# Optimization experiments

Measured on AMD Instinct MI355X. Metric: run time of the kernel, lower is better.

## Reference

```python
import math
import jax, jax.numpy as jnp
import numpy as np

B, L, E, H = 16, 4096, 512, 8
D = E // H
CORR_FACTOR = 2.0


def setup_inputs() -> dict:
    key = jax.random.key(0)
    ks = jax.random.split(key, 11)
    std = 1.0 / math.sqrt(E)
    mk = lambda k: (jax.random.normal(k, (E, E), jnp.float32) * std)
    return {
        "queries": jax.random.normal(ks[0], (B, L, E), jnp.float32),
        "keys": jax.random.normal(ks[1], (B, L, E), jnp.float32),
        "values": jax.random.normal(ks[2], (B, L, E), jnp.float32),
        "Wq": mk(ks[3]), "bq": jax.random.normal(ks[4], (E,), jnp.float32) * std,
        "Wk": mk(ks[5]), "bk": jax.random.normal(ks[6], (E,), jnp.float32) * std,
        "Wv": mk(ks[7]), "bv": jax.random.normal(ks[8], (E,), jnp.float32) * std,
        "Wo": mk(ks[9]), "bo": jax.random.normal(ks[10], (E,), jnp.float32) * std,
    }


def reference(queries, keys, values, Wq, bq, Wk, bk, Wv, bv, Wo, bo):
    # Projections (torch nn.Linear: x @ W.T + b), then split heads and move
    # to (B, H, D, L) layout used by the FFT / aggregation stages.
    def proj(x, W, b):
        y = x @ W.T + b                      # (B, L, E)
        return y.reshape(B, L, H, D).transpose(0, 2, 3, 1)  # (B, H, D, L)

    Q = proj(queries, Wq, bq)
    K = proj(keys, Wk, bk)
    V = proj(values, Wv, bv)

    # --- auto-correlation via Wiener-Khinchin (O(L log L)) ---
    qf = jnp.fft.rfft(Q, axis=-1)
    kf = jnp.fft.rfft(K, axis=-1)
    corr = jnp.fft.irfft(qf * jnp.conj(kf), n=L, axis=-1)  # (B, H, D, L)

    k_top = int(CORR_FACTOR * math.log(L))   # = 16
    corr_mean = jnp.mean(corr, axis=(1, 2))  # (B, L)
    top_vals, top_delays = jax.lax.top_k(corr_mean, k_top)  # (B, k)
    probs = jax.nn.softmax(top_vals, axis=-1)               # (B, k)

    pos = jnp.arange(L)
    agg = jnp.zeros_like(V)
    for i in range(k_top):  # small fixed loop over top-k delays
        idx = (pos[None, :] + top_delays[:, i:i + 1]) % L   # (B, L); == tiled gather
        v_del = jnp.take_along_axis(V, idx[:, None, None, :], axis=-1)
        agg = agg + probs[:, i, None, None, None] * v_del

    ctx = agg.transpose(0, 3, 1, 2).reshape(B, L, E)  # combine heads
    return ctx @ Wo.T + bo
```

## Files before the change

kernel.cpp:

```cpp
#include <hip/hip_runtime.h>
#include <hip/hip_bf16.h>
#include <math.h>


#define B_ 16
#define L_ 4096
#define E_ 512
#define NCAND 18
#define KTOP 16

typedef __attribute__((ext_vector_type(8))) short bf16x8;
typedef __attribute__((ext_vector_type(4))) float f32x4;

__device__ __forceinline__ float2 cmul(float2 a, float2 b) {
  return make_float2(a.x*b.x - a.y*b.y, a.x*b.y + a.y*b.x);
}
__device__ __forceinline__ float2 cadd(float2 a, float2 b){return make_float2(a.x+b.x, a.y+b.y);}
__device__ __forceinline__ float2 csub(float2 a, float2 b){return make_float2(a.x-b.x, a.y-b.y);}
__device__ __forceinline__ float2 cnegi(float2 a){return make_float2(a.y, -a.x);}
__device__ __forceinline__ unsigned short bf16_rne(float x) {
  unsigned int u = __float_as_uint(x);
  unsigned int r = u + 0x7FFFu + ((u >> 16) & 1u);
  return (unsigned short)(r >> 16);
}
__device__ __forceinline__ float bf16_f(unsigned short h) {
  return __uint_as_float(((unsigned int)h) << 16);
}

__device__ __forceinline__ void dft4(float2 a, float2 b, float2 c, float2 d,
                                     float2& X0, float2& X1, float2& X2, float2& X3) {
  float2 t0 = cadd(a,c), t1 = csub(a,c), t2 = cadd(b,d), t3 = csub(b,d);
  X0 = cadd(t0, t2); X2 = csub(t0, t2);
  float2 it3 = cnegi(t3);
  X1 = cadd(t1, it3);
  X3 = csub(t1, it3);
}

__device__ __forceinline__ void dft16(float2* v) {
  float2 B[4][4];
#pragma unroll
  for (int p = 0; p < 4; ++p)
    dft4(v[p], v[p+4], v[p+8], v[p+12], B[p][0], B[p][1], B[p][2], B[p][3]);
  const float C1 = 0.92387953251128674f, S1 = 0.38268343236508978f;
  const float C2 = 0.70710678118654752f;
  B[1][1] = cmul(B[1][1], make_float2( C1, -S1));
  B[1][2] = cmul(B[1][2], make_float2( C2, -C2));
  B[1][3] = cmul(B[1][3], make_float2( S1, -C1));
  B[2][1] = cmul(B[2][1], make_float2( C2, -C2));
  B[2][2] = cnegi(B[2][2]);
  B[2][3] = cmul(B[2][3], make_float2(-C2, -C2));
  B[3][1] = cmul(B[3][1], make_float2( S1, -C1));
  B[3][2] = cmul(B[3][2], make_float2(-C2, -C2));
  B[3][3] = cmul(B[3][3], make_float2(-C1,  S1));
#pragma unroll
  for (int r = 0; r < 4; ++r)
    dft4(B[0][r], B[1][r], B[2][r], B[3][r], v[r], v[r+4], v[r+8], v[r+12]);
}

__device__ __forceinline__ void fft4096_stages(float2* buf, int tid,
                                               const float2* __restrict__ tw) {
  float2 z[16];
#pragma unroll
  for (int q = 0; q < 16; ++q) z[q] = buf[tid + 256*q];
  __syncthreads();
  dft16(z);
  {
    const int p = tid, pa = tid & 15;
    buf[p*16 + (0 ^ pa)] = z[0];
#pragma unroll
    for (int r = 1; r < 16; ++r)
      buf[p*16 + (r ^ pa)] = cmul(z[r], tw[p*r]);
  }
  __syncthreads();
  {
    const int a = tid >> 4, r = tid & 15;
    float2 v[16];
#pragma unroll
    for (int bb = 0; bb < 16; ++bb) v[bb] = buf[(a + 16*bb)*16 + (r ^ a)];
    __syncthreads();
    dft16(v);
    buf[a*256 + 0*16 + r] = v[0];
#pragma unroll
    for (int c = 1; c < 16; ++c)
      buf[a*256 + c*16 + r] = cmul(v[c], tw[16*a*c]);
  }
  __syncthreads();
  {
    float2 y[16];
#pragma unroll
    for (int a = 0; a < 16; ++a) y[a] = buf[256*a + tid];
    __syncthreads();
    dft16(y);
#pragma unroll
    for (int d = 0; d < 16; ++d) buf[tid + 256*d] = y[d];
  }
  __syncthreads();
}

template<bool SPLIT>
__global__ __launch_bounds__(256) void conv_tile(
    const float* __restrict__ Xsrc,
    unsigned short* __restrict__ Thi, unsigned short* __restrict__ Tlo)
{
  const int bx = blockIdx.x;
  const int t  = blockIdx.y;
  const int tid = threadIdx.x;
  const int r = tid >> 1;
  const int h = tid & 1;
  const float* src = Xsrc + ((size_t)(bx*128 + r))*512 + t*32 + h*16;
  float xa[16];
#pragma unroll
  for (int q = 0; q < 4; ++q) {
    float4 v = *reinterpret_cast<const float4*>(src + 4*q);
    xa[4*q+0]=v.x; xa[4*q+1]=v.y; xa[4*q+2]=v.z; xa[4*q+3]=v.w;
  }
  size_t base = ((size_t)(bx*16 + t))*4096;
#pragma unroll
  for (int c = 0; c < 2; ++c) {
    int lk = h*2 + c;
    bf16x8 vh, vl;
#pragma unroll
    for (int e = 0; e < 8; ++e) {
      unsigned short hh = bf16_rne(xa[c*8+e]);
      vh[e] = (short)hh;
      if (SPLIT) vl[e] = (short)bf16_rne(xa[c*8+e] - bf16_f(hh));
    }
    *reinterpret_cast<bf16x8*>(Thi + base + ((size_t)lk*128 + r)*8) = vh;
    if (SPLIT)
      *reinterpret_cast<bf16x8*>(Tlo + base + ((size_t)lk*128 + r)*8) = vl;
  }
}

__global__ __launch_bounds__(256, 4) void gemm_qk(
    const float* __restrict__ Xq, const float* __restrict__ Xk,
    const unsigned short* __restrict__ Wqhi, const unsigned short* __restrict__ Wqlo,
    const unsigned short* __restrict__ Wkhi, const unsigned short* __restrict__ Wklo,
    const float* __restrict__ bq, const float* __restrict__ bk,
    float* __restrict__ Yq, float* __restrict__ Yk)
{
  __shared__ unsigned short Xh[2][2048], Xl[2][2048];
  const int sel = blockIdx.z;
  const float* X = sel ? Xk : Xq;
  const unsigned short* Whi = sel ? Wkhi : Wqhi;
  const unsigned short* Wlo = sel ? Wklo : Wqlo;
  const float* bias = sel ? bk : bq;
  float* Y = sel ? Yk : Yq;

  const int tid  = threadIdx.x;
  const int ny   = blockIdx.x;
  const int lt   = blockIdx.y;
  const int wave = tid >> 6;
  const int lane = tid & 63;
  const int lr   = lane & 15;
  const int lk   = lane >> 4;
  const int n0   = ny*256 + wave*64;
  const int cr   = tid >> 2;
  const int ch   = tid & 3;
  const int t0   = ((lt << 1) | ny) & 15;

  f32x4 acc[4][4];
#pragma unroll
  for (int i = 0; i < 4; ++i)
#pragma unroll
    for (int j = 0; j < 4; ++j) acc[i][j] = (f32x4){0.f,0.f,0.f,0.f};

  const float* Xb = X + ((size_t)(lt*64 + cr))*512 + ch*8;

  for (int it = 0; it < 16; ++it) {
    const int t = (t0 + it) & 15;
    const int p = it & 1;
    {
      float4 v0 = *reinterpret_cast<const float4*>(Xb + t*32);
      float4 v1 = *reinterpret_cast<const float4*>(Xb + t*32 + 4);
      float xa[8] = {v0.x,v0.y,v0.z,v0.w,v1.x,v1.y,v1.z,v1.w};
      bf16x8 vh, vl;
#pragma unroll
      for (int e = 0; e < 8; ++e) {
        unsigned short hh = bf16_rne(xa[e]);
        vh[e] = (short)hh;
        vl[e] = (short)bf16_rne(xa[e] - bf16_f(hh));
      }
      int u = (ch*64 + cr) ^ (ch*2);
      *reinterpret_cast<bf16x8*>(&Xh[p][u*8]) = vh;
      *reinterpret_cast<bf16x8*>(&Xl[p][u*8]) = vl;
    }
    bf16x8 ah[4], al[4];
#pragma unroll
    for (int i = 0; i < 4; ++i) {
      int n = n0 + i*16 + lr;
      size_t o = ((size_t)((n>>7)*16 + t))*4096 + ((size_t)lk*128 + (n&127))*8;
      ah[i] = *reinterpret_cast<const bf16x8*>(Whi + o);
      al[i] = *reinterpret_cast<const bf16x8*>(Wlo + o);
    }
    __syncthreads();

    __builtin_amdgcn_s_setprio(1);
#pragma unroll
    for (int j = 0; j < 4; ++j) {
      int u = (lk*64 + (j*16 + lr)) ^ (lk*2);
      bf16x8 bh = *reinterpret_cast<const bf16x8*>(&Xh[p][u*8]);
      bf16x8 bl = *reinterpret_cast<const bf16x8*>(&Xl[p][u*8]);
#pragma unroll
      for (int i = 0; i < 4; ++i) {
        acc[i][j] = __builtin_amdgcn_mfma_f32_16x16x32_bf16(ah[i], bh, acc[i][j], 0, 0, 0);
        acc[i][j] = __builtin_amdgcn_mfma_f32_16x16x32_bf16(ah[i], bl, acc[i][j], 0, 0, 0);
        acc[i][j] = __builtin_amdgcn_mfma_f32_16x16x32_bf16(al[i], bh, acc[i][j], 0, 0, 0);
      }
    }
    __builtin_amdgcn_s_setprio(0);
  }

  const int bb = lt >> 6;
  const int lbase = (lt & 63)*64;
#pragma unroll
  for (int i = 0; i < 4; ++i) {
    int n = n0 + i*16 + lk*4;
#pragma unroll
    for (int j = 0; j < 4; ++j) {
      int l = lbase + j*16 + lr;
#pragma unroll
      for (int r = 0; r < 4; ++r) {
        Y[((size_t)(bb*512 + n + r))*4096 + l] = acc[i][j][r] + bias[n + r];
      }
    }
  }
}

__global__ __launch_bounds__(512) void gemm_ov(
    const float* __restrict__ V, const unsigned short* __restrict__ Wct,
    const float* __restrict__ bias, unsigned short* __restrict__ Y16)
{
  __shared__ unsigned short Vs[2][256*8];
  const int tid  = threadIdx.x;
  const int bx   = blockIdx.x;
  const int wave = tid >> 6;
  const int lane = tid & 63;
  const int lr   = lane & 15;
  const int lk   = lane >> 4;
  const int n0   = wave*64;
  const int cr   = tid >> 3;
  const int ch   = tid & 7;
  const int clk  = ch >> 1;
  const int chh  = ch & 1;
  const int coff = (((clk*64 + cr) ^ clk)*8 + chh*4);
  const int t0   = bx & 15;

  f32x4 acc[4][4];
#pragma unroll
  for (int i = 0; i < 4; ++i)
#pragma unroll
    for (int j = 0; j < 4; ++j) acc[i][j] = (f32x4){0.f,0.f,0.f,0.f};

  const float* Vb = V + (size_t)bx*64*512 + (size_t)cr*512 + ch*4;
  float4 xv = *reinterpret_cast<const float4*>(Vb + t0*32);

  for (int it = 0; it < 16; ++it) {
    const int t = (t0 + it) & 15;
    const int p = it & 1;
    uint2 hi2 = make_uint2(
        (unsigned)bf16_rne(xv.x) | ((unsigned)bf16_rne(xv.y) << 16),
        (unsigned)bf16_rne(xv.z) | ((unsigned)bf16_rne(xv.w) << 16));
    *reinterpret_cast<uint2*>(&Vs[p][coff]) = hi2;
    float4 xnext;
    if (it < 15) {
      int tn = (t0 + it + 1) & 15;
      xnext = *reinterpret_cast<const float4*>(Vb + tn*32);
    }
    __syncthreads();

    bf16x8 av[4];
#pragma unroll
    for (int i = 0; i < 4; ++i) {
      int u = ((lk*64 + i*16 + lr) ^ lk)*8;
      av[i] = *reinterpret_cast<const bf16x8*>(&Vs[p][u]);
    }
#pragma unroll
    for (int j = 0; j < 4; ++j) {
      int n = n0 + j*16 + lr;
      size_t o = ((size_t)((n>>7)*16 + t))*4096 + ((size_t)lk*128 + (n&127))*8;
      bf16x8 bw = *reinterpret_cast<const bf16x8*>(Wct + o);
#pragma unroll
      for (int i = 0; i < 4; ++i)
        acc[i][j] = __builtin_amdgcn_mfma_f32_16x16x32_bf16(av[i], bw, acc[i][j], 0, 0, 0);
    }
    if (it < 15) xv = xnext;
  }

#pragma unroll
  for (int i = 0; i < 4; ++i) {
#pragma unroll
    for (int j = 0; j < 4; ++j) {
      int n = n0 + j*16 + lr;
      float bs = bias[n];
#pragma unroll
      for (int r = 0; r < 4; ++r) {
        int m = bx*64 + i*16 + lk*4 + r;
        Y16[(size_t)m*512 + n] = bf16_rne(acc[i][j][r] + bs);
      }
    }
  }
}

__global__ __launch_bounds__(256) void combine_kernel(
    const float* __restrict__ Wo, const float* __restrict__ Wv,
    const float* __restrict__ bv, const float* __restrict__ bo,
    float* __restrict__ Wc, float* __restrict__ bc)
{
  int n = blockIdx.x;
  int tid = threadIdx.x;
  float a0 = 0.f, a1 = 0.f;
  for (int j = 0; j < 512; ++j) {
    float wo = Wo[(size_t)n*512 + j];
    a0 += wo * Wv[(size_t)j*512 + tid];
    a1 += wo * Wv[(size_t)j*512 + tid + 256];
  }
  Wc[(size_t)n*512 + tid]       = a0;
  Wc[(size_t)n*512 + tid + 256] = a1;

  float p = 0.f;
  for (int j = tid; j < 512; j += 256) p += Wo[(size_t)n*512 + j] * bv[j];
  __shared__ float red[256];
  red[tid] = p; __syncthreads();
  for (int off = 128; off > 0; off >>= 1) {
    if (tid < off) red[tid] += red[tid + off];
    __syncthreads();
  }
  if (tid == 0) bc[n] = red[0] + bo[n];
}

__global__ void init_tw_kernel(float2* __restrict__ tw) {
  int k = blockIdx.x * 256 + threadIdx.x;
  if (k < 4096) {
    double ang = -2.0 * M_PI * (double)k / 4096.0;
    tw[k] = make_float2((float)cos(ang), (float)sin(ang));
  }
}

template<int CHB>
__global__ __launch_bounds__(256) void fft_corr_kernel(
    const float* __restrict__ Qt, const float* __restrict__ Kt,
    const float2* __restrict__ tw, float2* __restrict__ Spart)
{
  __shared__ float2 buf[4096];
  const int NG = 512 / CHB;
  const int b = blockIdx.x / NG;
  const int g = blockIdx.x % NG;
  const int tid = threadIdx.x;

  float2 acc[16];
#pragma unroll
  for (int m = 0; m < 16; ++m) acc[m] = make_float2(0.f, 0.f);

  float4 qv[4], kv[4];
  {
    const float* Qr = Qt + ((size_t)b*512 + g*CHB) * 4096;
    const float* Kr = Kt + ((size_t)b*512 + g*CHB) * 4096;
#pragma unroll
    for (int j = 0; j < 4; ++j) {
      qv[j] = *reinterpret_cast<const float4*>(Qr + 4*(tid + 256*j));
      kv[j] = *reinterpret_cast<const float4*>(Kr + 4*(tid + 256*j));
    }
  }

  for (int cc = 0; cc < CHB; ++cc) {
#pragma unroll
    for (int j = 0; j < 4; ++j) {
      int l0 = 4*(tid + 256*j);
      buf[l0+0] = make_float2(qv[j].x, kv[j].x);
      buf[l0+1] = make_float2(qv[j].y, kv[j].y);
      buf[l0+2] = make_float2(qv[j].z, kv[j].z);
      buf[l0+3] = make_float2(qv[j].w, kv[j].w);
    }
    __syncthreads();
    if (cc + 1 < CHB) {
      const float* Qr = Qt + ((size_t)b*512 + g*CHB + cc + 1) * 4096;
      const float* Kr = Kt + ((size_t)b*512 + g*CHB + cc + 1) * 4096;
#pragma unroll
      for (int j = 0; j < 4; ++j) {
        qv[j] = *reinterpret_cast<const float4*>(Qr + 4*(tid + 256*j));
        kv[j] = *reinterpret_cast<const float4*>(Kr + 4*(tid + 256*j));
      }
    }

    fft4096_stages(buf, tid, tw);

#pragma unroll
    for (int m = 0; m < 16; ++m) {
      int f = tid + 256*m;
      float2 zf = buf[f];
      float2 zm = buf[(4096 - f) & 4095];
      float2 qf = make_float2(0.5f*(zf.x + zm.x), 0.5f*(zf.y - zm.y));
      float2 df = make_float2(0.5f*(zf.x - zm.x), 0.5f*(zf.y + zm.y));
      float2 kf = make_float2(df.y, -df.x);
      acc[m].x += qf.x*kf.x + qf.y*kf.y;
      acc[m].y += qf.y*kf.x - qf.x*kf.y;
    }
    __syncthreads();
  }
  float2* Sp = Spart + ((size_t)(b*NG + g)) * 4096;
#pragma unroll
  for (int m = 0; m < 16; ++m) Sp[tid + 256*m] = acc[m];
}

__global__ __launch_bounds__(256) void reduce_spart_kernel(
    const float2* __restrict__ Spart, float2* __restrict__ S, int ng)
{
  const int b  = blockIdx.x >> 4;
  const int f  = ((blockIdx.x & 15) << 8) | threadIdx.x;
  float sx = 0.f, sy = 0.f;
  const float2* base = Spart + (size_t)b * ng * 4096 + f;
  for (int g = 0; g < ng; ++g) {
    float2 v = base[(size_t)g * 4096];
    sx += v.x; sy += v.y;
  }
  S[(size_t)b*4096 + f] = make_float2(sx, -sy);
}

__global__ __launch_bounds__(256) void ifft_kernel(
    const float2* __restrict__ S, const float2* __restrict__ tw,
    float* __restrict__ corr)
{
  __shared__ float2 buf[4096];
  const int b = blockIdx.x;
  const int tid = threadIdx.x;
#pragma unroll
  for (int m = 0; m < 16; ++m) {
    int f = tid + 256*m;
    buf[f] = S[(size_t)b*4096 + f];
  }
  __syncthreads();
  fft4096_stages(buf, tid, tw);
  const float scale = 1.0f / (512.0f * 4096.0f);
#pragma unroll
  for (int m = 0; m < 16; ++m) {
    int t = tid + 256*m;
    corr[(size_t)b*4096 + t] = buf[t].x * scale;
  }
}

__global__ __launch_bounds__(256) void topk_kernel(
    const float* __restrict__ corr, float* __restrict__ cand_val,
    int* __restrict__ cand_idx, int* __restrict__ flags)
{
  __shared__ float vals[4096];
  __shared__ float rv[256];
  __shared__ int   ri[256];
  const int b = blockIdx.x;
  const int tid = threadIdx.x;
#pragma unroll
  for (int r = 0; r < 16; ++r) vals[tid + 256*r] = corr[(size_t)b*4096 + tid + 256*r];
  __syncthreads();

  for (int it = 0; it < NCAND; ++it) {
    float best = -1e30f; int bi = -1;
#pragma unroll
    for (int r = 0; r < 16; ++r) {
      int i = tid + 256*r;
      float v = vals[i];
      if (v > best) { best = v; bi = i; }
    }
    rv[tid] = best; ri[tid] = bi;
    __syncthreads();
    for (int off = 128; off > 0; off >>= 1) {
      if (tid < off) {
        float v2 = rv[tid + off]; int i2 = ri[tid + off];
        if (v2 > rv[tid] || (v2 == rv[tid] && i2 < ri[tid])) { rv[tid] = v2; ri[tid] = i2; }
      }
      __syncthreads();
    }
    if (tid == 0) {
      cand_val[b*NCAND + it] = rv[0];
      cand_idx[b*NCAND + it] = ri[0];
      vals[ri[0]] = -1e30f;
    }
    __syncthreads();
  }
  if (tid == 0)
    flags[b] = (cand_val[b*NCAND + 15] - cand_val[b*NCAND + 16] < 0.012f) ? 1 : 0;
}

__global__ __launch_bounds__(256) void refine_kernel(
    const float* __restrict__ Qt, const float* __restrict__ Kt,
    const int* __restrict__ cand_idx, const int* __restrict__ flags,
    float* __restrict__ refpart)
{
  const int b = blockIdx.x >> 5;
  const int chunk = blockIdx.x & 31;
  if (!flags[b]) return;
  __shared__ float Qs[4096];
  __shared__ float red[4*NCAND];
  const int tid = threadIdx.x;
  int taus[NCAND];
#pragma unroll
  for (int i = 0; i < NCAND; ++i) taus[i] = cand_idx[b*NCAND + i];
  float acc[NCAND];
#pragma unroll
  for (int i = 0; i < NCAND; ++i) acc[i] = 0.f;

  for (int cc = 0; cc < 16; ++cc) {
    int c = chunk*16 + cc;
    const float* Qc = Qt + ((size_t)b*512 + c)*4096;
    const float* Kc = Kt + ((size_t)b*512 + c)*4096;
    __syncthreads();
#pragma unroll
    for (int rr = 0; rr < 4; ++rr) {
      int l4 = (tid + 256*rr)*4;
      *reinterpret_cast<float4*>(&Qs[l4]) = *reinterpret_cast<const float4*>(Qc + l4);
    }
    __syncthreads();
#pragma unroll 2
    for (int j = 0; j < 16; ++j) {
      int l = tid + 256*j;
      float kv = Kc[l];
#pragma unroll
      for (int i = 0; i < NCAND; ++i)
        acc[i] += Qs[(l + taus[i]) & 4095] * kv;
    }
  }
#pragma unroll
  for (int i = 0; i < NCAND; ++i) {
    float v = acc[i];
    for (int off = 32; off > 0; off >>= 1) v += __shfl_down(v, off);
    if ((tid & 63) == 0) red[(tid >> 6)*NCAND + i] = v;
  }
  __syncthreads();
  if (tid < NCAND) {
    float s = red[tid] + red[NCAND + tid] + red[2*NCAND + tid] + red[3*NCAND + tid];
    refpart[(size_t)(b*32 + chunk)*NCAND + tid] = s;
  }
}

__global__ void finalize_kernel(const float* __restrict__ refpart,
                                const int* __restrict__ flags,
                                float* __restrict__ cand_val)
{
  int b = blockIdx.x;
  if (!flags[b]) return;
  int i = threadIdx.x;
  if (i >= NCAND) return;
  double s = 0.0;
  for (int g = 0; g < 32; ++g) s += (double)refpart[(size_t)(b*32 + g)*NCAND + i];
  cand_val[b*NCAND + i] = (float)(s / 512.0);
}

__global__ void probs_kernel(const float* __restrict__ cand_val,
                             const int* __restrict__ cand_idx,
                             float* __restrict__ probs, int* __restrict__ delays)
{
  int b = blockIdx.x;
  if (threadIdx.x != 0) return;
  float v[NCAND]; int ix[NCAND]; bool used[NCAND];
  for (int i = 0; i < NCAND; ++i) {
    v[i] = cand_val[b*NCAND + i]; ix[i] = cand_idx[b*NCAND + i]; used[i] = false;
  }
  float sel_v[KTOP]; int sel_i[KTOP];
  for (int k = 0; k < KTOP; ++k) {
    int best = -1;
    for (int i = 0; i < NCAND; ++i) {
      if (used[i]) continue;
      if (best < 0 || v[i] > v[best] || (v[i] == v[best] && ix[i] < ix[best])) best = i;
    }
    used[best] = true; sel_v[k] = v[best]; sel_i[k] = ix[best];
  }
  float mx = sel_v[0];
  for (int k = 1; k < KTOP; ++k) mx = fmaxf(mx, sel_v[k]);
  float e[KTOP]; float se = 0.f;
  for (int k = 0; k < KTOP; ++k) { e[k] = __expf(sel_v[k] - mx); se += e[k]; }
  for (int k = 0; k < KTOP; ++k) {
    probs[b*KTOP + k]  = e[k] / se;
    delays[b*KTOP + k] = sel_i[k];
  }
}

__global__ __launch_bounds__(256) void agg_kernel(
    const unsigned short* __restrict__ OV, const float* __restrict__ probs,
    const int* __restrict__ delays, float* __restrict__ out, int bbase)
{
  int b  = bbase + (blockIdx.x & 7);
  int l  = (blockIdx.x >> 3) * 4 + (threadIdx.x >> 6);
  int c8 = (threadIdx.x & 63) << 3;
  float p[KTOP]; int d[KTOP];
#pragma unroll
  for (int i = 0; i < KTOP; ++i) { p[i] = probs[b*KTOP + i]; d[i] = delays[b*KTOP + i]; }
  float acc[8];
#pragma unroll
  for (int j = 0; j < 8; ++j) acc[j] = 0.f;
#pragma unroll
  for (int i = 0; i < KTOP; ++i) {
    int ls = (l + d[i]) & 4095;
    uint4 v = *reinterpret_cast<const uint4*>(OV + ((size_t)((b << 12) | ls))*512 + c8);
    unsigned int uu[4] = {v.x, v.y, v.z, v.w};
    float pi = p[i];
#pragma unroll
    for (int t = 0; t < 4; ++t) {
      acc[2*t]   += pi * __uint_as_float(uu[t] << 16);
      acc[2*t+1] += pi * __uint_as_float(uu[t] & 0xFFFF0000u);
    }
  }
  float* dst = out + ((size_t)((b << 12) | l))*512 + c8;
  *reinterpret_cast<float4*>(dst)     = make_float4(acc[0], acc[1], acc[2], acc[3]);
  *reinterpret_cast<float4*>(dst + 4) = make_float4(acc[4], acc[5], acc[6], acc[7]);
}

extern "C" void kernel_launch(void* const* d_in, const int* in_sizes, int n_in,
                              void* d_out, int out_size, void* d_ws, size_t ws_size,
                              hipStream_t stream)
{
  const float* queries = (const float*)d_in[0];
  const float* keys    = (const float*)d_in[1];
  const float* values  = (const float*)d_in[2];
  const float* Wq = (const float*)d_in[3];
  const float* bq = (const float*)d_in[4];
  const float* Wk = (const float*)d_in[5];
  const float* bk = (const float*)d_in[6];
  const float* Wv = (const float*)d_in[7];
  const float* bv = (const float*)d_in[8];
  const float* Wo = (const float*)d_in[9];
  const float* bo = (const float*)d_in[10];

  const size_t WT = (size_t)E_*E_*2;
  const size_t fixed = (size_t)B_*E_*L_*4
                     + (size_t)B_*L_*8
                     + (size_t)B_*L_*4
                     + (size_t)E_*E_*4 + E_*4
                     + (size_t)4096*8
                     + (size_t)B_*NCAND*8 + B_*4
                     + (size_t)B_*KTOP*8
                     + (size_t)B_*32*NCAND*4
                     + 5*WT;
  const int NG = (ws_size >= fixed + (size_t)B_*64*L_*8) ? 64 : 32;

  char* ws = (char*)d_ws;
  size_t off = 0;
  float* Qt   = (float*)(ws + off);    off += (size_t)B_*E_*L_*4;
  float2* Spart = (float2*)(ws + off); off += (size_t)B_*NG*L_*8;
  float2* S   = (float2*)(ws + off);   off += (size_t)B_*L_*8;
  float* corr = (float*)(ws + off);    off += (size_t)B_*L_*4;
  float* Wc   = (float*)(ws + off);    off += (size_t)E_*E_*4;
  float* bc   = (float*)(ws + off);    off += (size_t)E_*4;
  float2* tw  = (float2*)(ws + off);   off += (size_t)4096*8;
  float* cand_val = (float*)(ws + off); off += (size_t)B_*NCAND*4;
  int*   cand_idx = (int*)(ws + off);   off += (size_t)B_*NCAND*4;
  int*   flags    = (int*)(ws + off);   off += (size_t)B_*4;
  float* probs    = (float*)(ws + off); off += (size_t)B_*KTOP*4;
  int*   delays   = (int*)(ws + off);   off += (size_t)B_*KTOP*4;
  float* refpart  = (float*)(ws + off); off += (size_t)B_*32*NCAND*4;
  unsigned short* Wqhi = (unsigned short*)(ws + off); off += WT;
  unsigned short* Wqlo = (unsigned short*)(ws + off); off += WT;
  unsigned short* Wkhi = (unsigned short*)(ws + off); off += WT;
  unsigned short* Wklo = (unsigned short*)(ws + off); off += WT;
  unsigned short* Wcthi = (unsigned short*)(ws + off); off += WT;

  float* Kt = (float*)d_out;
  unsigned short* OV = (unsigned short*)Qt;

  init_tw_kernel<<<16, 256, 0, stream>>>(tw);
  conv_tile<true><<<dim3(4,16), 256, 0, stream>>>(Wq, Wqhi, Wqlo);
  conv_tile<true><<<dim3(4,16), 256, 0, stream>>>(Wk, Wkhi, Wklo);
  combine_kernel<<<E_, 256, 0, stream>>>(Wo, Wv, bv, bo, Wc, bc);
  conv_tile<false><<<dim3(4,16), 256, 0, stream>>>(Wc, Wcthi, Wcthi);

  gemm_qk<<<dim3(2, 1024, 2), 256, 0, stream>>>(queries, keys, Wqhi, Wqlo, Wkhi, Wklo,
                                                bq, bk, Qt, Kt);

  if (NG == 64)
    fft_corr_kernel<8><<<B_*64, 256, 0, stream>>>(Qt, Kt, tw, Spart);
  else
    fft_corr_kernel<16><<<B_*32, 256, 0, stream>>>(Qt, Kt, tw, Spart);
  reduce_spart_kernel<<<B_*16, 256, 0, stream>>>(Spart, S, NG);
  ifft_kernel<<<B_, 256, 0, stream>>>(S, tw, corr);
  topk_kernel<<<B_, 256, 0, stream>>>(corr, cand_val, cand_idx, flags);
  refine_kernel<<<B_*32, 256, 0, stream>>>(Qt, Kt, cand_idx, flags, refpart);
  finalize_kernel<<<B_, 32, 0, stream>>>(refpart, flags, cand_val);
  probs_kernel<<<B_, 64, 0, stream>>>(cand_val, cand_idx, probs, delays);

  gemm_ov<<<1024, 512, 0, stream>>>(values, Wcthi, bc, OV);
  agg_kernel<<<8192, 256, 0, stream>>>(OV, probs, delays, (float*)d_out, 0);
  agg_kernel<<<8192, 256, 0, stream>>>(OV, probs, delays, (float*)d_out, 8);
}
```

Measured before the change: 754.0 us.

## Split QK GEMM launches, reorder MFMAs, restructure OV loads, add NG=128 FFT path

Splits the fused Q/K projection GEMM into two separate launches and reorders its MFMA chain so the four independent accumulators are interleaved per pass rather than chained back-to-back. The OV GEMM drops the register prefetch of V in favour of loading V and all four weight fragments before the barrier, and gains a min-blocks launch bound. A new NG=128 configuration for the FFT correlation kernel is used when the workspace is large enough, giving more blocks with fewer channels each. The changes trade extra partial-sum memory and reduction work, plus register pressure from the launch bound, for more parallelism and less MFMA dependency stall.

After: 824.0 us. +9.3%, slower.

```diff
diff --git a/kernel.cpp b/kernel.cpp
--- a/kernel.cpp
+++ b/kernel.cpp
@@ -132,20 +132,11 @@
 }
 
 __global__ __launch_bounds__(256, 4) void gemm_qk(
-    const float* __restrict__ Xq, const float* __restrict__ Xk,
-    const unsigned short* __restrict__ Wqhi, const unsigned short* __restrict__ Wqlo,
-    const unsigned short* __restrict__ Wkhi, const unsigned short* __restrict__ Wklo,
-    const float* __restrict__ bq, const float* __restrict__ bk,
-    float* __restrict__ Yq, float* __restrict__ Yk)
+    const float* __restrict__ X,
+    const unsigned short* __restrict__ Whi, const unsigned short* __restrict__ Wlo,
+    const float* __restrict__ bias, float* __restrict__ Y)
 {
   __shared__ unsigned short Xh[2][2048], Xl[2][2048];
-  const int sel = blockIdx.z;
-  const float* X = sel ? Xk : Xq;
-  const unsigned short* Whi = sel ? Wkhi : Wqhi;
-  const unsigned short* Wlo = sel ? Wklo : Wqlo;
-  const float* bias = sel ? bk : bq;
-  float* Y = sel ? Yk : Yq;
-
   const int tid  = threadIdx.x;
   const int ny   = blockIdx.x;
   const int lt   = blockIdx.y;
@@ -201,11 +192,14 @@
       bf16x8 bh = *reinterpret_cast<const bf16x8*>(&Xh[p][u*8]);
       bf16x8 bl = *reinterpret_cast<const bf16x8*>(&Xl[p][u*8]);
 #pragma unroll
-      for (int i = 0; i < 4; ++i) {
+      for (int i = 0; i < 4; ++i)
         acc[i][j] = __builtin_amdgcn_mfma_f32_16x16x32_bf16(ah[i], bh, acc[i][j], 0, 0, 0);
+#pragma unroll
+      for (int i = 0; i < 4; ++i)
         acc[i][j] = __builtin_amdgcn_mfma_f32_16x16x32_bf16(ah[i], bl, acc[i][j], 0, 0, 0);
+#pragma unroll
+      for (int i = 0; i < 4; ++i)
         acc[i][j] = __builtin_amdgcn_mfma_f32_16x16x32_bf16(al[i], bh, acc[i][j], 0, 0, 0);
-      }
     }
     __builtin_amdgcn_s_setprio(0);
   }
@@ -226,7 +220,7 @@
   }
 }
 
-__global__ __launch_bounds__(512) void gemm_ov(
+__global__ __launch_bounds__(512, 4) void gemm_ov(
     const float* __restrict__ V, const unsigned short* __restrict__ Wct,
     const float* __restrict__ bias, unsigned short* __restrict__ Y16)
 {
@@ -252,19 +246,23 @@
     for (int j = 0; j < 4; ++j) acc[i][j] = (f32x4){0.f,0.f,0.f,0.f};
 
   const float* Vb = V + (size_t)bx*64*512 + (size_t)cr*512 + ch*4;
-  float4 xv = *reinterpret_cast<const float4*>(Vb + t0*32);
 
   for (int it = 0; it < 16; ++it) {
     const int t = (t0 + it) & 15;
     const int p = it & 1;
-    uint2 hi2 = make_uint2(
-        (unsigned)bf16_rne(xv.x) | ((unsigned)bf16_rne(xv.y) << 16),
-        (unsigned)bf16_rne(xv.z) | ((unsigned)bf16_rne(xv.w) << 16));
-    *reinterpret_cast<uint2*>(&Vs[p][coff]) = hi2;
-    float4 xnext;
-    if (it < 15) {
-      int tn = (t0 + it + 1) & 15;
-      xnext = *reinterpret_cast<const float4*>(Vb + tn*32);
+    {
+      float4 xv = *reinterpret_cast<const float4*>(Vb + t*32);
+      uint2 hi2 = make_uint2(
+          (unsigned)bf16_rne(xv.x) | ((unsigned)bf16_rne(xv.y) << 16),
+          (unsigned)bf16_rne(xv.z) | ((unsigned)bf16_rne(xv.w) << 16));
+      *reinterpret_cast<uint2*>(&Vs[p][coff]) = hi2;
+    }
+    bf16x8 bw[4];
+#pragma unroll
+    for (int j = 0; j < 4; ++j) {
+      int n = n0 + j*16 + lr;
+      size_t o = ((size_t)((n>>7)*16 + t))*4096 + ((size_t)lk*128 + (n&127))*8;
+      bw[j] = *reinterpret_cast<const bf16x8*>(Wct + o);
     }
     __syncthreads();
 
@@ -275,15 +273,10 @@
       av[i] = *reinterpret_cast<const bf16x8*>(&Vs[p][u]);
     }
 #pragma unroll
-    for (int j = 0; j < 4; ++j) {
-      int n = n0 + j*16 + lr;
-      size_t o = ((size_t)((n>>7)*16 + t))*4096 + ((size_t)lk*128 + (n&127))*8;
-      bf16x8 bw = *reinterpret_cast<const bf16x8*>(Wct + o);
+    for (int j = 0; j < 4; ++j)
 #pragma unroll
       for (int i = 0; i < 4; ++i)
-        acc[i][j] = __builtin_amdgcn_mfma_f32_16x16x32_bf16(av[i], bw, acc[i][j], 0, 0, 0);
-    }
-    if (it < 15) xv = xnext;
+        acc[i][j] = __builtin_amdgcn_mfma_f32_16x16x32_bf16(av[i], bw[j], acc[i][j], 0, 0, 0);
   }
 
 #pragma unroll
@@ -628,7 +621,10 @@
                      + (size_t)B_*KTOP*8
                      + (size_t)B_*32*NCAND*4
                      + 5*WT;
-  const int NG = (ws_size >= fixed + (size_t)B_*64*L_*8) ? 64 : 32;
+  int NG;
+  if (ws_size >= fixed + (size_t)B_*128*L_*8)      NG = 128;
+  else if (ws_size >= fixed + (size_t)B_*64*L_*8)  NG = 64;
+  else                                             NG = 32;
 
   char* ws = (char*)d_ws;
   size_t off = 0;
@@ -660,10 +656,12 @@
   combine_kernel<<<E_, 256, 0, stream>>>(Wo, Wv, bv, bo, Wc, bc);
   conv_tile<false><<<dim3(4,16), 256, 0, stream>>>(Wc, Wcthi, Wcthi);
 
-  gemm_qk<<<dim3(2, 1024, 2), 256, 0, stream>>>(queries, keys, Wqhi, Wqlo, Wkhi, Wklo,
-                                                bq, bk, Qt, Kt);
-
-  if (NG == 64)
+  gemm_qk<<<dim3(2, 1024), 256, 0, stream>>>(queries, Wqhi, Wqlo, bq, Qt);
+  gemm_qk<<<dim3(2, 1024), 256, 0, stream>>>(keys,    Wkhi, Wklo, bk, Kt);
+
+  if (NG == 128)
+    fft_corr_kernel<4><<<B_*128, 256, 0, stream>>>(Qt, Kt, tw, Spart);
+  else if (NG == 64)
     fft_corr_kernel<8><<<B_*64, 256, 0, stream>>>(Qt, Kt, tw, Spart);
   else
     fft_corr_kernel<16><<<B_*32, 256, 0, stream>>>(Qt, Kt, tw, Spart);
```
